# Kernel optimization log

Measured on AMD Instinct MI355X. Metric: run time of the kernel, lower is better.

The kernel has to match this reference:

```python
import jax, jax.numpy as jnp
import numpy as np

B, NUM_VN, NUM_CN, D = 4, 65536, 32768, 32
DEG = 8
E = NUM_CN * DEG  # 262144 edges per side
HID, MSG = 40, 20


def setup_inputs() -> dict:
    key = jax.random.key(0)
    ks = jax.random.split(key, 16)
    inp = {
        "h_from": jax.random.normal(ks[0], (B, NUM_VN, D), jnp.float32),
        "h_to_x": jax.random.normal(ks[1], (B, NUM_CN, D), jnp.float32),
        "h_to_z": jax.random.normal(ks[2], (B, NUM_CN, D), jnp.float32),
        "hx_logit": jax.random.normal(ks[3], (B, NUM_CN), jnp.float32),
        "hz_logit": jax.random.normal(ks[4], (B, NUM_CN), jnp.float32),
        "from_ind_x": jax.random.randint(ks[5], (E,), 0, NUM_VN, jnp.int32),
        "to_ind_x": jax.random.randint(ks[6], (E,), 0, NUM_CN, jnp.int32),
        "from_ind_z": jax.random.randint(ks[7], (E,), 0, NUM_VN, jnp.int32),
        "to_ind_z": jax.random.randint(ks[8], (E,), 0, NUM_CN, jnp.int32),
        # msg MLP: in 2*D -> HID -> MSG ; embed MLP: in MSG+D+1 -> HID -> D
        "Wm1_x": jax.random.normal(ks[9], (2 * D, HID), jnp.float32) * 0.1,
        "Wm2_x": jax.random.normal(ks[10], (HID, MSG), jnp.float32) * 0.1,
        "Wm1_z": jax.random.normal(ks[11], (2 * D, HID), jnp.float32) * 0.1,
        "Wm2_z": jax.random.normal(ks[12], (HID, MSG), jnp.float32) * 0.1,
        "We1_x": jax.random.normal(ks[13], (MSG + D + 1, HID), jnp.float32) * 0.1,
        "We2_x": jax.random.normal(ks[14], (HID, D), jnp.float32) * 0.1,
        "We1_z": jax.random.normal(ks[15], (MSG + D + 1, HID), jnp.float32) * 0.1,
        "We2_z": jax.random.normal(jax.random.fold_in(key, 99), (HID, D), jnp.float32) * 0.1,
    }
    return inp


def _side(h_from, h_to, logit, from_ind, to_ind, Wm1, Wm2, We1, We2):
    # gather edge endpoint embeddings: [B, E, 2*D]
    feat = jnp.concatenate([h_from[:, from_ind], h_to[:, to_ind]], axis=-1)
    # per-edge message MLP (relu hidden, linear out, no bias): [B, E, MSG]
    msg = jax.nn.relu(feat @ Wm1) @ Wm2
    # segment-sum aggregation onto receiving check nodes: [B, NUM_CN, MSG]
    n_cn = h_to.shape[1]
    m = jnp.zeros((h_to.shape[0], n_cn, msg.shape[-1]), msg.dtype).at[:, to_ind].add(msg)
    # embedding update MLP on [m, h_to, logit]: [B, NUM_CN, D]
    emb_in = jnp.concatenate([m, h_to, logit[..., None]], axis=-1)
    return jax.nn.relu(emb_in @ We1) @ We2


def reference(h_from, h_to_x, h_to_z, hx_logit, hz_logit,
              from_ind_x, to_ind_x, from_ind_z, to_ind_z,
              Wm1_x, Wm2_x, Wm1_z, Wm2_z, We1_x, We2_x, We1_z, We2_z):
    h_to_x_new = _side(h_from, h_to_x, hx_logit, from_ind_x, to_ind_x,
                       Wm1_x, Wm2_x, We1_x, We2_x)
    h_to_z_new = _side(h_from, h_to_z, hz_logit, from_ind_z, to_ind_z,
                       Wm1_z, Wm2_z, We1_z, We2_z)
    return (h_to_x_new, h_to_z_new)
```

## Files before the change

### kernel.cpp

```cpp
#include <hip/hip_runtime.h>
#include <hip/hip_bf16.h>

#define NVN 65536
#define NCN 32768
#define NB 4
#define DIM 32
#define NE 262144
#define HID 40
#define MSGD 20
#define SLOT 40

typedef unsigned short u16;
typedef unsigned int u32;
typedef __attribute__((ext_vector_type(8))) short bf16x8;
typedef __attribute__((ext_vector_type(4))) float f32x4;

__device__ __forceinline__ u16 f2bf(float f) {
    __hip_bfloat16 h = __float2bfloat16(f);
    return *reinterpret_cast<u16*>(&h);
}
__device__ __forceinline__ u32 pk2(float a, float b) {
    __hip_bfloat162 h = __float22bfloat162_rn(float2{a, b});
    return *reinterpret_cast<u32*>(&h);
}
__device__ __forceinline__ float bflo(u32 u) { return __uint_as_float(u << 16); }
__device__ __forceinline__ float bfhi(u32 u) { return __uint_as_float(u & 0xffff0000u); }


__device__ __forceinline__ void repack_lines(int tid, const u16* sOut, u16* dst, int v0) {
    const u32* so = (const u32*)sOut;
    uint4* dp = (uint4*)((char*)dst + (size_t)v0 * 320);
    for (int i = tid; i < 640; i += 256) {
        int vloc = i / 20;
        int q0 = (i - vloc * 20) * 4;
        u32 vals[4];
#pragma unroll
        for (int j = 0; j < 4; j++) {
            int q = q0 + j;
            int ch, cp;
            if (q < 32)      { ch = q >> 2;        cp = (ch >> 2) * 10 + (q & 3); }
            else if (q < 64) { int t = q - 32; ch = t >> 2; cp = (ch >> 2) * 10 + 4 + (t & 3); }
            else             { int t = q - 64; ch = t >> 1; cp = (ch >> 2) * 10 + 8 + (t & 1); }
            int m = (ch & 3) * 32 + vloc;
            vals[j] = so[m * 20 + cp];
        }
        dp[i] = make_uint4(vals[0], vals[1], vals[2], vals[3]);
    }
}


__device__ __forceinline__ void precompU_both_body(
        int bidl, int tid, const float* __restrict__ h_from,
        const float* __restrict__ Wx, const float* __restrict__ Wz,
        u16* __restrict__ dstx, u16* __restrict__ dstz,
        u16* sA, u16* sB, u16* sOut) {
    int v0 = bidl << 5;

    for (int i = tid; i < 2 * 1536; i += 256) {
        int sd = (i >= 1536);
        int idx = sd ? i - 1536 : i;
        int row = idx / 48, col = idx - row * 48;
        const float* W = sd ? Wz : Wx;
        sB[i] = (col < 40) ? f2bf(W[row * 40 + col]) : (u16)0;
    }
    {
        int r = tid >> 1, p = tid & 1;
        int b = r >> 5, vloc = r & 31;
        const float4* hp = (const float4*)(h_from + ((size_t)b * NVN + v0 + vloc) * DIM + p * 16);
        float4 x0 = hp[0], x1 = hp[1], x2 = hp[2], x3 = hp[3];
        uint4* d = (uint4*)(sA + r * 32 + p * 16);
        d[0] = make_uint4(pk2(x0.x, x0.y), pk2(x0.z, x0.w), pk2(x1.x, x1.y), pk2(x1.z, x1.w));
        d[1] = make_uint4(pk2(x2.x, x2.y), pk2(x2.z, x2.w), pk2(x3.x, x3.y), pk2(x3.z, x3.w));
    }
    __syncthreads();

    int wid = tid >> 6;
    int lane = tid & 63;
    int li = lane & 15;
    int lk = lane >> 4;

    bf16x8 bfr[2][3];
#pragma unroll
    for (int s = 0; s < 2; s++)
#pragma unroll
        for (int jt = 0; jt < 3; jt++) {
            bf16x8 v;
#pragma unroll
            for (int rr = 0; rr < 8; rr++)
                v[rr] = (short)sB[s * 1536 + (lk * 8 + rr) * 48 + jt * 16 + li];
            bfr[s][jt] = v;
        }
    bf16x8 a0 = *(const bf16x8*)(sA + (wid * 32 + li) * 32 + lk * 8);
    bf16x8 a1 = *(const bf16x8*)(sA + (wid * 32 + 16 + li) * 32 + lk * 8);

#pragma unroll
    for (int s = 0; s < 2; s++) {
        if (s) __syncthreads();
#pragma unroll
        for (int rt = 0; rt < 2; rt++) {
            int rowloc = wid * 32 + rt * 16;
            bf16x8 a = rt ? a1 : a0;
#pragma unroll
            for (int jt = 0; jt < 3; jt++) {
                f32x4 acc = {0.f, 0.f, 0.f, 0.f};
                acc = __builtin_amdgcn_mfma_f32_16x16x32_bf16(a, bfr[s][jt], acc, 0, 0, 0);
                int col = jt * 16 + li;
                if (col < 40) {
#pragma unroll
                    for (int rr = 0; rr < 4; rr++)
                        sOut[(rowloc + lk * 4 + rr) * 40 + col] = f2bf(acc[rr]);
                }
            }
        }
        __syncthreads();
        repack_lines(tid, sOut, s ? dstz : dstx, v0);
    }
}


__device__ __forceinline__ void precompT_body(
        int bidl, int tid,
        const float* __restrict__ h_x, const float* __restrict__ h_z,
        const float* __restrict__ W_x, const float* __restrict__ W_z,
        u16* __restrict__ dst_x, u16* __restrict__ dst_z,
        u16* sA, u16* sB, u16* sOut) {
    int bps = NCN >> 5;
    int side = bidl / bps;
    int v0 = (bidl - side * bps) << 5;

    const float* __restrict__ h = side ? h_z : h_x;
    const float* __restrict__ W = side ? W_z : W_x;
    u16* dst = side ? dst_z : dst_x;

    for (int i = tid; i < 1536; i += 256) {
        int row = i / 48, col = i - row * 48;
        sB[i] = (col < 40) ? f2bf(W[row * 40 + col]) : (u16)0;
    }
    {
        int r = tid >> 1, p = tid & 1;
        int b = r >> 5, vloc = r & 31;
        const float4* hp = (const float4*)(h + ((size_t)b * NCN + v0 + vloc) * DIM + p * 16);
        float4 x0 = hp[0], x1 = hp[1], x2 = hp[2], x3 = hp[3];
        uint4* d = (uint4*)(sA + r * 32 + p * 16);
        d[0] = make_uint4(pk2(x0.x, x0.y), pk2(x0.z, x0.w), pk2(x1.x, x1.y), pk2(x1.z, x1.w));
        d[1] = make_uint4(pk2(x2.x, x2.y), pk2(x2.z, x2.w), pk2(x3.x, x3.y), pk2(x3.z, x3.w));
    }
    __syncthreads();

    int wid = tid >> 6;
    int lane = tid & 63;
    int li = lane & 15;
    int lk = lane >> 4;

    bf16x8 bfr[3];
#pragma unroll
    for (int jt = 0; jt < 3; jt++) {
        bf16x8 v;
#pragma unroll
        for (int rr = 0; rr < 8; rr++)
            v[rr] = (short)sB[(lk * 8 + rr) * 48 + jt * 16 + li];
        bfr[jt] = v;
    }

#pragma unroll
    for (int rt = 0; rt < 2; rt++) {
        int rowloc = wid * 32 + rt * 16;
        bf16x8 a = *(const bf16x8*)(sA + (rowloc + li) * 32 + lk * 8);
#pragma unroll
        for (int jt = 0; jt < 3; jt++) {
            f32x4 acc = {0.f, 0.f, 0.f, 0.f};
            acc = __builtin_amdgcn_mfma_f32_16x16x32_bf16(a, bfr[jt], acc, 0, 0, 0);
            int col = jt * 16 + li;
            if (col < 40) {
#pragma unroll
                for (int rr = 0; rr < 4; rr++)
                    sOut[(rowloc + lk * 4 + rr) * 40 + col] = f2bf(acc[rr]);
            }
        }
    }
    __syncthreads();
    repack_lines(tid, sOut, dst, v0);
}


__global__ __launch_bounds__(256) void phase1(
        const int* __restrict__ to_x, const int* __restrict__ from_x,
        const int* __restrict__ to_z, const int* __restrict__ from_z,
        int* __restrict__ cnt_x, int* __restrict__ cnt_z,
        u16* __restrict__ ef_x, u16* __restrict__ ef_z,
        const float* __restrict__ h_from,
        const float* __restrict__ h_to_x, const float* __restrict__ h_to_z,
        const float* __restrict__ Wm1_x, const float* __restrict__ Wm1_z,
        const float* __restrict__ Wm2_x, const float* __restrict__ Wm2_z,
        const float* __restrict__ We1_x, const float* __restrict__ We1_z,
        const float* __restrict__ We2_x, const float* __restrict__ We2_z,
        u16* __restrict__ U2h_x, u16* __restrict__ U2h_z,
        u16* __restrict__ ts_x, u16* __restrict__ ts_z,
        u16* __restrict__ BW_x, u16* __restrict__ BW_z,
        u16* __restrict__ W2_x, u16* __restrict__ W2_z) {
    __shared__ __attribute__((aligned(16))) u16 sA[128 * 32];
    __shared__ __attribute__((aligned(16))) u16 sB[2 * 1536];
    __shared__ __attribute__((aligned(16))) u16 sOut[128 * 40];

    int bid = blockIdx.x;
    int tid = threadIdx.x;

    if (bid < 2048) {
        int e = (bid & 1023) * 256 + tid;
        const int* t; const int* f; int* cnt; u16* ef;
        if (bid < 1024) { t = to_x; f = from_x; cnt = cnt_x; ef = ef_x; }
        else            { t = to_z; f = from_z; cnt = cnt_z; ef = ef_z; }
        int c = t[e];
        int pos = atomicAdd(&cnt[c], 1);
        if (pos < SLOT) ef[c * SLOT + pos] = (u16)f[e];
    } else if (bid < 4096) {
        precompU_both_body(bid - 2048, tid, h_from, Wm1_x, Wm1_z,
                           U2h_x, U2h_z, sA, sB, sOut);
    } else if (bid < 6144) {
        precompT_body(bid - 4096, tid, h_to_x, h_to_z,
                      Wm1_x + DIM * HID, Wm1_z + DIM * HID,
                      ts_x, ts_z, sA, sB, sOut);
    } else {
        int side = bid - 6144;
        const float* Wm2 = side ? Wm2_z : Wm2_x;
        const float* We1 = side ? We1_z : We1_x;
        const float* We2 = side ? We2_z : We2_x;
        u16* BW = side ? BW_z : BW_x;
        u16* W2 = side ? W2_z : W2_x;
        for (int i = tid; i < 96 * 48; i += 256) {
            int row = i / 48, col = i % 48;
            float v = 0.f;
            if (col < 40) {
                if (row < 40) {
                    for (int k = 0; k < MSGD; k++) v += Wm2[row * MSGD + k] * We1[k * HID + col];
                } else if (row < 72) {
                    v = We1[(MSGD + row - 40) * HID + col];
                } else if (row == 72) {
                    v = We1[(MSGD + DIM) * HID + col];
                }
            }
            BW[i] = f2bf(v);
        }
        for (int i = tid; i < 64 * 32; i += 256) {
            int row = i / 32, col = i % 32;
            W2[i] = (row < 40) ? f2bf(We2[row * 32 + col]) : (u16)0;
        }
    }
}


__global__ __launch_bounds__(256, 8) void aggA_kernel(
        const u16* __restrict__ U2h_x, const u16* __restrict__ U2h_z,
        u16* __restrict__ ts_x, u16* __restrict__ ts_z,
        const int* __restrict__ cnt_x, const int* __restrict__ cnt_z,
        const u16* __restrict__ ef_x, const u16* __restrict__ ef_z) {
    int side = blockIdx.x >> 11;
    const char* Ubase = (const char*)(side ? U2h_z : U2h_x);
    char* ts = (char*)(side ? ts_z : ts_x);
    const int* cnt = side ? cnt_z : cnt_x;
    const u16* ef = side ? ef_z : ef_x;

    int gt = (blockIdx.x & 2047) * 256 + threadIdx.x;
    int c = gt >> 4;
    int l16 = gt & 15;
    int chunk = l16 & 7;
    int par = l16 >> 3;
    int off16a = chunk * 16;
    int off8c = 256 + chunk * 8;

    char* tline = ts + (size_t)c * 320;
    uint4 T0 = *(const uint4*)(tline + off16a);
    uint4 T1 = *(const uint4*)(tline + off16a + 128);
    uint2 Tc = *(const uint2*)(tline + off8c);

    float s[20];
#pragma unroll
    for (int k = 0; k < 20; k++) s[k] = 0.f;

    int cn = cnt[c];
    cn = (cn < SLOT) ? cn : SLOT;
    const u16* efc = ef + c * SLOT;

    int vA = (par < cn) ? (int)efc[par] : 0;
#define ACC(su, aw, tw) { \
    s[su]     += fmaxf(bflo(aw) + bflo(tw), 0.f); \
    s[(su)+1] += fmaxf(bfhi(aw) + bfhi(tw), 0.f); }
    for (int i = par; i < cn; i += 2) {
        const char* pa = Ubase + (size_t)vA * 320;
        uint4 A0 = *(const uint4*)(pa + off16a);
        uint4 A1 = *(const uint4*)(pa + off16a + 128);
        uint2 A2 = *(const uint2*)(pa + off8c);
        vA = (i + 2 < cn) ? (int)efc[i + 2] : 0;
        ACC(0, A0.x, T0.x)  ACC(2, A0.y, T0.y)  ACC(4, A0.z, T0.z)  ACC(6, A0.w, T0.w)
        ACC(8, A1.x, T1.x)  ACC(10, A1.y, T1.y) ACC(12, A1.z, T1.z) ACC(14, A1.w, T1.w)
        ACC(16, A2.x, Tc.x) ACC(18, A2.y, Tc.y)
    }
#undef ACC

#pragma unroll
    for (int k = 0; k < 20; k++) s[k] += __shfl_xor(s[k], 8);

    if (par == 0) {
        u32 sp[10];
#pragma unroll
        for (int jq = 0; jq < 5; jq++) {
            sp[2 * jq]     = pk2(s[4 * jq + 0], s[4 * jq + 1]);
            sp[2 * jq + 1] = pk2(s[4 * jq + 2], s[4 * jq + 3]);
        }
        *(uint4*)(tline + off16a)       = make_uint4(sp[0], sp[1], sp[2], sp[3]);
        *(uint4*)(tline + off16a + 128) = make_uint4(sp[4], sp[5], sp[6], sp[7]);
        *(uint2*)(tline + off8c)        = make_uint2(sp[8], sp[9]);
    }
}


__global__ __launch_bounds__(256) void aggB_mfma(
        const u16* __restrict__ ts_x, const u16* __restrict__ ts_z,
        const float* __restrict__ h_to_x, const float* __restrict__ h_to_z,
        const float* __restrict__ logit_x, const float* __restrict__ logit_z,
        const u16* __restrict__ BW_x, const u16* __restrict__ BW_z,
        const u16* __restrict__ W2_x, const u16* __restrict__ W2_z,
        float* __restrict__ out) {
    __shared__ __attribute__((aligned(16))) u16 sA[128 * 96];
    __shared__ __attribute__((aligned(16))) u16 sH[128 * 64];
    __shared__ __attribute__((aligned(16))) u16 sBW[96 * 48];
    __shared__ __attribute__((aligned(16))) u16 sW2[64 * 32];

    int bid = blockIdx.x;
    int side = bid >> 10;
    const u16* ts = side ? ts_z : ts_x;
    const float* h_to = side ? h_to_z : h_to_x;
    const float* logit = side ? logit_z : logit_x;
    const u16* BWg = side ? BW_z : BW_x;
    const u16* W2g = side ? W2_z : W2_x;

    int tid = threadIdx.x;
    int rho0 = (bid & 1023) * 128;
    int b = rho0 >> 15;
    int c0 = rho0 & 32767;

    for (int i = tid; i < (96 * 48) / 8; i += 256)
        ((uint4*)sBW)[i] = ((const uint4*)BWg)[i];
    if (tid < (64 * 32) / 8) ((uint4*)sW2)[tid] = ((const uint4*)W2g)[tid];

    {
        int r = tid >> 1;
        int part = tid & 1;
        int c = c0 + r;
        char* srow = (char*)sA + r * 192;
        if (part == 0) {
            const char* tr = (const char*)ts + (size_t)c * 320;
            uint4 p0 = *(const uint4*)(tr + b * 16);
            uint4 p1 = *(const uint4*)(tr + 128 + b * 16);
            uint2 p2 = *(const uint2*)(tr + 256 + b * 8);
            uint4 p3 = *(const uint4*)(tr + (4 + b) * 16);
            uint4 p4 = *(const uint4*)(tr + 128 + (4 + b) * 16);
            uint2 p5 = *(const uint2*)(tr + 256 + (4 + b) * 8);
            *(uint4*)(srow + 0)  = p0;
            *(uint4*)(srow + 16) = p1;
            *(uint2*)(srow + 32) = p2;
            *(uint2*)(srow + 40) = make_uint2(p3.x, p3.y);
            *(uint2*)(srow + 48) = make_uint2(p3.z, p3.w);
            *(uint2*)(srow + 56) = make_uint2(p4.x, p4.y);
            *(uint2*)(srow + 64) = make_uint2(p4.z, p4.w);
            *(uint2*)(srow + 72) = p5;
            char* hrow = (char*)sH + r * 128;
            *(uint4*)(hrow + 96)  = make_uint4(0, 0, 0, 0);
            *(uint4*)(hrow + 112) = make_uint4(0, 0, 0, 0);
        } else {
            const float4* xp = (const float4*)(h_to + ((size_t)b * NCN + c) * DIM);
#pragma unroll
            for (int q = 0; q < 4; q++) {
                float4 x0 = xp[2 * q], x1 = xp[2 * q + 1];
                *(uint4*)(srow + 80 + q * 16) =
                    make_uint4(pk2(x0.x, x0.y), pk2(x0.z, x0.w),
                               pk2(x1.x, x1.y), pk2(x1.z, x1.w));
            }
            float lg = logit[(size_t)b * NCN + c];
            *(uint4*)(srow + 144) = make_uint4((u32)f2bf(lg), 0, 0, 0);
            *(uint4*)(srow + 160) = make_uint4(0, 0, 0, 0);
            *(uint4*)(srow + 176) = make_uint4(0, 0, 0, 0);
        }
    }
    __syncthreads();

    int wid = tid >> 6;
    int lane = tid & 63;
    int li = lane & 15;
    int lk = lane >> 4;
    int rowq = lk * 4;

    bf16x8 bA[3][3];
#pragma unroll
    for (int jt = 0; jt < 3; jt++)
#pragma unroll
        for (int ks = 0; ks < 3; ks++) {
            bf16x8 v;
#pragma unroll
            for (int rr = 0; rr < 8; rr++)
                v[rr] = (short)sBW[(ks * 32 + lk * 8 + rr) * 48 + jt * 16 + li];
            bA[jt][ks] = v;
        }

#pragma unroll
    for (int rt = 0; rt < 2; rt++) {
        int rowloc = wid * 32 + rt * 16;
        const char* abase = (const char*)sA + (rowloc + li) * 192 + lk * 16;
        bf16x8 a0 = *(const bf16x8*)(abase);
        bf16x8 a1 = *(const bf16x8*)(abase + 64);
        bf16x8 a2 = *(const bf16x8*)(abase + 128);
#pragma unroll
        for (int jt = 0; jt < 3; jt++) {
            f32x4 acc = {0.f, 0.f, 0.f, 0.f};
            acc = __builtin_amdgcn_mfma_f32_16x16x32_bf16(a0, bA[jt][0], acc, 0, 0, 0);
            acc = __builtin_amdgcn_mfma_f32_16x16x32_bf16(a1, bA[jt][1], acc, 0, 0, 0);
            acc = __builtin_amdgcn_mfma_f32_16x16x32_bf16(a2, bA[jt][2], acc, 0, 0, 0);
#pragma unroll
            for (int rr = 0; rr < 4; rr++)
                sH[(rowloc + rowq + rr) * 64 + jt * 16 + li] = f2bf(fmaxf(acc[rr], 0.f));
        }
    }
    __syncthreads();

    bf16x8 bB[2][2];
#pragma unroll
    for (int jt = 0; jt < 2; jt++)
#pragma unroll
        for (int ks = 0; ks < 2; ks++) {
            bf16x8 v;
#pragma unroll
            for (int rr = 0; rr < 8; rr++)
                v[rr] = (short)sW2[(ks * 32 + lk * 8 + rr) * 32 + jt * 16 + li];
            bB[jt][ks] = v;
        }

    size_t rowg0 = (size_t)bid * 128;
#pragma unroll
    for (int rt = 0; rt < 2; rt++) {
        int rowloc = wid * 32 + rt * 16;
        const char* hbase = (const char*)sH + (rowloc + li) * 128 + lk * 16;
        bf16x8 h0 = *(const bf16x8*)(hbase);
        bf16x8 h1 = *(const bf16x8*)(hbase + 64);
#pragma unroll
        for (int jt = 0; jt < 2; jt++) {
            f32x4 acc = {0.f, 0.f, 0.f, 0.f};
            acc = __builtin_amdgcn_mfma_f32_16x16x32_bf16(h0, bB[jt][0], acc, 0, 0, 0);
            acc = __builtin_amdgcn_mfma_f32_16x16x32_bf16(h1, bB[jt][1], acc, 0, 0, 0);
#pragma unroll
            for (int rr = 0; rr < 4; rr++)
                out[(rowg0 + rowloc + rowq + rr) * 32 + jt * 16 + li] = acc[rr];
        }
    }
}


extern "C" void kernel_launch(void* const* d_in, const int* in_sizes, int n_in,
                              void* d_out, int out_size, void* d_ws, size_t ws_size,
                              hipStream_t stream) {
    const float* h_from   = (const float*)d_in[0];
    const float* h_to_x   = (const float*)d_in[1];
    const float* h_to_z   = (const float*)d_in[2];
    const float* hx_logit = (const float*)d_in[3];
    const float* hz_logit = (const float*)d_in[4];
    const int*   from_x   = (const int*)d_in[5];
    const int*   to_x     = (const int*)d_in[6];
    const int*   from_z   = (const int*)d_in[7];
    const int*   to_z     = (const int*)d_in[8];
    const float* Wm1_x    = (const float*)d_in[9];
    const float* Wm2_x    = (const float*)d_in[10];
    const float* Wm1_z    = (const float*)d_in[11];
    const float* Wm2_z    = (const float*)d_in[12];
    const float* We1_x    = (const float*)d_in[13];
    const float* We2_x    = (const float*)d_in[14];
    const float* We1_z    = (const float*)d_in[15];
    const float* We2_z    = (const float*)d_in[16];

    char* ws = (char*)d_ws;
    u16* U2h_x = (u16*)(ws);
    u16* U2h_z = (u16*)(ws + 20971520);
    u16* ts_x  = (u16*)(ws + 41943040);
    u16* ts_z  = (u16*)(ws + 52428800);
    u16* ef_x  = (u16*)(ws + 62914560);
    u16* ef_z  = (u16*)(ws + 65536000);
    int* cnt_x = (int*)(ws + 68157440);
    int* cnt_z = (int*)(ws + 68288512);
    u16* BW_x  = (u16*)(ws + 68419584);
    u16* BW_z  = (u16*)(ws + 68428800);
    u16* W2_x  = (u16*)(ws + 68438016);
    u16* W2_z  = (u16*)(ws + 68442112);
    float* out = (float*)d_out;

    hipMemsetAsync(ws + 68157440, 0, 262144, stream);
    phase1<<<6146, 256, 0, stream>>>(to_x, from_x, to_z, from_z,
                                     cnt_x, cnt_z, ef_x, ef_z,
                                     h_from, h_to_x, h_to_z,
                                     Wm1_x, Wm1_z, Wm2_x, Wm2_z,
                                     We1_x, We1_z, We2_x, We2_z,
                                     U2h_x, U2h_z, ts_x, ts_z,
                                     BW_x, BW_z, W2_x, W2_z);
    aggA_kernel<<<4096, 256, 0, stream>>>(U2h_x, U2h_z, ts_x, ts_z,
                                          cnt_x, cnt_z, ef_x, ef_z);
    aggB_mfma<<<2048, 256, 0, stream>>>(ts_x, ts_z, h_to_x, h_to_z,
                                        hx_logit, hz_logit,
                                        BW_x, BW_z, W2_x, W2_z, out);
}
```

Before: 126.6 us.

## Store precomputed per-node hidden tables in blocked row-major layout

Replaces the interleaved 320-byte per-node line layout with a blocked layout: 32 nodes per 10 KB block, each batch holding a contiguous 80-byte row per node. The precompute kernels can then copy the MFMA output from shared memory directly instead of running a permutation repack. aggA gathers five 8-byte pieces per lane instead of two 16-byte loads plus one 8-byte load, and aggB reads five contiguous 16-byte vectors per row. The trade-off is narrower, less coalesced gather loads in the edge aggregation loop, which could raise memory transactions on the random-access path.

```diff
diff --git a/kernel.cpp b/kernel.cpp
--- a/kernel.cpp
+++ b/kernel.cpp
@@ -27,25 +27,11 @@
 __device__ __forceinline__ float bfhi(u32 u) { return __uint_as_float(u & 0xffff0000u); }
 
 
-__device__ __forceinline__ void repack_lines(int tid, const u16* sOut, u16* dst, int v0) {
-    const u32* so = (const u32*)sOut;
-    uint4* dp = (uint4*)((char*)dst + (size_t)v0 * 320);
-    for (int i = tid; i < 640; i += 256) {
-        int vloc = i / 20;
-        int q0 = (i - vloc * 20) * 4;
-        u32 vals[4];
-#pragma unroll
-        for (int j = 0; j < 4; j++) {
-            int q = q0 + j;
-            int ch, cp;
-            if (q < 32)      { ch = q >> 2;        cp = (ch >> 2) * 10 + (q & 3); }
-            else if (q < 64) { int t = q - 32; ch = t >> 2; cp = (ch >> 2) * 10 + 4 + (t & 3); }
-            else             { int t = q - 64; ch = t >> 1; cp = (ch >> 2) * 10 + 8 + (t & 1); }
-            int m = (ch & 3) * 32 + vloc;
-            vals[j] = so[m * 20 + cp];
-        }
-        dp[i] = make_uint4(vals[0], vals[1], vals[2], vals[3]);
-    }
+
+__device__ __forceinline__ void copy_lines(int tid, const u16* sOut, u16* dst, int vblk) {
+    const uint4* so = (const uint4*)sOut;
+    uint4* dp = (uint4*)((char*)dst + (size_t)vblk * 10240);
+    for (int i = tid; i < 640; i += 256) dp[i] = so[i];
 }
 
 
@@ -113,7 +99,7 @@
             }
         }
         __syncthreads();
-        repack_lines(tid, sOut, s ? dstz : dstx, v0);
+        copy_lines(tid, sOut, s ? dstz : dstx, bidl);
     }
 }
 
@@ -126,7 +112,8 @@
         u16* sA, u16* sB, u16* sOut) {
     int bps = NCN >> 5;
     int side = bidl / bps;
-    int v0 = (bidl - side * bps) << 5;
+    int vblk = bidl - side * bps;
+    int v0 = vblk << 5;
 
     const float* __restrict__ h = side ? h_z : h_x;
     const float* __restrict__ W = side ? W_z : W_x;
@@ -179,7 +166,7 @@
         }
     }
     __syncthreads();
-    repack_lines(tid, sOut, dst, v0);
+    copy_lines(tid, sOut, dst, vblk);
 }
 
 
@@ -265,13 +252,16 @@
     int l16 = gt & 15;
     int chunk = l16 & 7;
     int par = l16 >> 3;
-    int off16a = chunk * 16;
-    int off8c = 256 + chunk * 8;
-
-    char* tline = ts + (size_t)c * 320;
-    uint4 T0 = *(const uint4*)(tline + off16a);
-    uint4 T1 = *(const uint4*)(tline + off16a + 128);
-    uint2 Tc = *(const uint2*)(tline + off8c);
+    int b = chunk & 3;
+    int half = chunk >> 2;
+    int coff = b * 2560 + half * 40;
+
+    char* tline = ts + (size_t)(c >> 5) * 10240 + (c & 31) * 80 + coff;
+    uint2 T0 = *(const uint2*)(tline + 0);
+    uint2 T1 = *(const uint2*)(tline + 8);
+    uint2 T2 = *(const uint2*)(tline + 16);
+    uint2 T3 = *(const uint2*)(tline + 24);
+    uint2 T4 = *(const uint2*)(tline + 32);
 
     float s[20];
 #pragma unroll
@@ -282,20 +272,22 @@
     const u16* efc = ef + c * SLOT;
 
     int vA = (par < cn) ? (int)efc[par] : 0;
-#define ACC(su, aw, tw) { \
-    s[su]     += fmaxf(bflo(aw) + bflo(tw), 0.f); \
-    s[(su)+1] += fmaxf(bfhi(aw) + bfhi(tw), 0.f); }
+#define ACC2(su, aw, tw) { \
+    s[su]     += fmaxf(bflo(aw.x) + bflo(tw.x), 0.f); \
+    s[(su)+1] += fmaxf(bfhi(aw.x) + bfhi(tw.x), 0.f); \
+    s[(su)+2] += fmaxf(bflo(aw.y) + bflo(tw.y), 0.f); \
+    s[(su)+3] += fmaxf(bfhi(aw.y) + bfhi(tw.y), 0.f); }
     for (int i = par; i < cn; i += 2) {
-        const char* pa = Ubase + (size_t)vA * 320;
-        uint4 A0 = *(const uint4*)(pa + off16a);
-        uint4 A1 = *(const uint4*)(pa + off16a + 128);
-        uint2 A2 = *(const uint2*)(pa + off8c);
+        const char* pa = Ubase + (size_t)(vA >> 5) * 10240 + (vA & 31) * 80 + coff;
+        uint2 A0 = *(const uint2*)(pa + 0);
+        uint2 A1 = *(const uint2*)(pa + 8);
+        uint2 A2 = *(const uint2*)(pa + 16);
+        uint2 A3 = *(const uint2*)(pa + 24);
+        uint2 A4 = *(const uint2*)(pa + 32);
         vA = (i + 2 < cn) ? (int)efc[i + 2] : 0;
-        ACC(0, A0.x, T0.x)  ACC(2, A0.y, T0.y)  ACC(4, A0.z, T0.z)  ACC(6, A0.w, T0.w)
-        ACC(8, A1.x, T1.x)  ACC(10, A1.y, T1.y) ACC(12, A1.z, T1.z) ACC(14, A1.w, T1.w)
-        ACC(16, A2.x, Tc.x) ACC(18, A2.y, Tc.y)
-    }
-#undef ACC
+        ACC2(0, A0, T0) ACC2(4, A1, T1) ACC2(8, A2, T2) ACC2(12, A3, T3) ACC2(16, A4, T4)
+    }
+#undef ACC2
 
 #pragma unroll
     for (int k = 0; k < 20; k++) s[k] += __shfl_xor(s[k], 8);
@@ -307,9 +299,11 @@
             sp[2 * jq]     = pk2(s[4 * jq + 0], s[4 * jq + 1]);
             sp[2 * jq + 1] = pk2(s[4 * jq + 2], s[4 * jq + 3]);
         }
-        *(uint4*)(tline + off16a)       = make_uint4(sp[0], sp[1], sp[2], sp[3]);
-        *(uint4*)(tline + off16a + 128) = make_uint4(sp[4], sp[5], sp[6], sp[7]);
-        *(uint2*)(tline + off8c)        = make_uint2(sp[8], sp[9]);
+        *(uint2*)(tline + 0)  = make_uint2(sp[0], sp[1]);
+        *(uint2*)(tline + 8)  = make_uint2(sp[2], sp[3]);
+        *(uint2*)(tline + 16) = make_uint2(sp[4], sp[5]);
+        *(uint2*)(tline + 24) = make_uint2(sp[6], sp[7]);
+        *(uint2*)(tline + 32) = make_uint2(sp[8], sp[9]);
     }
 }
 
@@ -349,21 +343,14 @@
         int c = c0 + r;
         char* srow = (char*)sA + r * 192;
         if (part == 0) {
-            const char* tr = (const char*)ts + (size_t)c * 320;
-            uint4 p0 = *(const uint4*)(tr + b * 16);
-            uint4 p1 = *(const uint4*)(tr + 128 + b * 16);
-            uint2 p2 = *(const uint2*)(tr + 256 + b * 8);
-            uint4 p3 = *(const uint4*)(tr + (4 + b) * 16);
-            uint4 p4 = *(const uint4*)(tr + 128 + (4 + b) * 16);
-            uint2 p5 = *(const uint2*)(tr + 256 + (4 + b) * 8);
-            *(uint4*)(srow + 0)  = p0;
-            *(uint4*)(srow + 16) = p1;
-            *(uint2*)(srow + 32) = p2;
-            *(uint2*)(srow + 40) = make_uint2(p3.x, p3.y);
-            *(uint2*)(srow + 48) = make_uint2(p3.z, p3.w);
-            *(uint2*)(srow + 56) = make_uint2(p4.x, p4.y);
-            *(uint2*)(srow + 64) = make_uint2(p4.z, p4.w);
-            *(uint2*)(srow + 72) = p5;
+            const uint4* tr = (const uint4*)((const char*)ts
+                    + (size_t)(c >> 5) * 10240 + b * 2560 + (c & 31) * 80);
+            uint4 q0 = tr[0], q1 = tr[1], q2 = tr[2], q3 = tr[3], q4 = tr[4];
+            *(uint4*)(srow + 0)  = q0;
+            *(uint4*)(srow + 16) = q1;
+            *(uint4*)(srow + 32) = q2;
+            *(uint4*)(srow + 48) = q3;
+            *(uint4*)(srow + 64) = q4;
             char* hrow = (char*)sH + r * 128;
             *(uint4*)(hrow + 96)  = make_uint4(0, 0, 0, 0);
             *(uint4*)(hrow + 112) = make_uint4(0, 0, 0, 0);
```

New measurement: 144.8 us, median of 2. +14.4%, slower.
